# Performance work log

Hardware: AMD Instinct MI355X
Metric: run time of the kernel (lower is better)

The kernel has to match this reference:

```python
import jax, jax.numpy as jnp
import numpy as np

H, D = 4, 128          # num_heads, per-head out dim (= hidden_feats)
IN = 256               # input feature dim for both node types
N_HOST, N_FLOW = 100000, 100000
E1, E2 = 200000, 200000  # edges for host->flow ('h2f') and flow->host ('f2h')
LN_EPS = 1e-5
SLOPE = 0.2            # GATConv default LeakyReLU negative_slope


def setup_inputs() -> dict:
    key = jax.random.key(0)
    ks = jax.random.split(key, 16)
    nrm = lambda k, s, sc=0.05: jax.random.normal(k, s, jnp.float32) * sc
    return {
        'feat_host': jax.random.normal(ks[0], (N_HOST, IN), jnp.float32),
        'feat_flow': jax.random.normal(ks[1], (N_FLOW, IN), jnp.float32),
        # GATConv params for rel h2f (src=host, dst=flow)
        'W1': nrm(ks[2], (IN, H * D)), 'al1': nrm(ks[3], (H, D)), 'ar1': nrm(ks[4], (H, D)), 'b1': jnp.zeros((H * D,), jnp.float32),
        # GATConv params for rel f2h (src=flow, dst=host)
        'W2': nrm(ks[5], (IN, H * D)), 'al2': nrm(ks[6], (H, D)), 'ar2': nrm(ks[7], (H, D)), 'b2': jnp.zeros((H * D,), jnp.float32),
        # residual projections (in_feats 256 != hidden 128)
        'projW_host': nrm(ks[8], (IN, D)), 'projb_host': jnp.zeros((D,), jnp.float32),
        'projW_flow': nrm(ks[9], (IN, D)), 'projb_flow': jnp.zeros((D,), jnp.float32),
        # LayerNorm params
        'g_host': jnp.ones((D,), jnp.float32), 'be_host': jnp.zeros((D,), jnp.float32),
        'g_flow': jnp.ones((D,), jnp.float32), 'be_flow': jnp.zeros((D,), jnp.float32),
        # edge lists
        'e1_src': jax.random.randint(ks[10], (E1,), 0, N_HOST, jnp.int32),
        'e1_dst': jax.random.randint(ks[11], (E1,), 0, N_FLOW, jnp.int32),
        'e2_src': jax.random.randint(ks[12], (E2,), 0, N_FLOW, jnp.int32),
        'e2_dst': jax.random.randint(ks[13], (E2,), 0, N_HOST, jnp.int32),
    }


def _gat_rel(h_src, h_dst, src, dst, W, al, ar, b, n_dst):
    """DGL GATConv (shared fc, residual=False, bias=True, eval-mode dropout)."""
    fs = (h_src @ W).reshape(-1, H, D)                     # [Ns,H,D]
    fd = (h_dst @ W).reshape(-1, H, D)                     # [Nd,H,D]
    el = jnp.sum(fs * al, axis=-1)                         # [Ns,H]
    er = jnp.sum(fd * ar, axis=-1)                         # [Nd,H]
    e = jax.nn.leaky_relu(el[src] + er[dst], SLOPE)        # [E,H]
    # edge softmax over incoming edges of each dst node (per head), max-stabilized
    m = jax.ops.segment_max(e, dst, num_segments=n_dst)    # [Nd,H]
    ee = jnp.exp(e - m[dst])
    s = jax.ops.segment_sum(ee, dst, num_segments=n_dst)   # [Nd,H]
    a = ee / s[dst]                                        # [E,H]
    msg = a[:, :, None] * fs[src]                          # [E,H,D]
    rst = jax.ops.segment_sum(msg, dst, num_segments=n_dst)  # [Nd,H,D]
    return rst + b.reshape(H, D)


def _tail(agg, feat, pW, pb, g, be):
    """mean over heads -> residual(projected) -> LayerNorm -> GELU (dropout=eval)."""
    h = agg.mean(axis=1)                                   # [N,D]
    c = h + (feat @ pW + pb)
    mu = c.mean(axis=-1, keepdims=True)
    var = ((c - mu) ** 2).mean(axis=-1, keepdims=True)
    y = (c - mu) / jnp.sqrt(var + LN_EPS) * g + be
    return jax.nn.gelu(y, approximate=False)


def reference(feat_host, feat_flow, W1, al1, ar1, b1, W2, al2, ar2, b2,
              projW_host, projb_host, projW_flow, projb_flow,
              g_host, be_host, g_flow, be_flow,
              e1_src, e1_dst, e2_src, e2_dst):
    flow_agg = _gat_rel(feat_host, feat_flow, e1_src, e1_dst, W1, al1, ar1, b1, N_FLOW)
    host_agg = _gat_rel(feat_flow, feat_host, e2_src, e2_dst, W2, al2, ar2, b2, N_HOST)
    host_out = _tail(host_agg, feat_host, projW_host, projb_host, g_host, be_host)
    flow_out = _tail(flow_agg, feat_flow, projW_flow, projb_flow, g_flow, be_flow)
    return host_out, flow_out
```

## Files before the change

kernel.cpp:

```cpp
#include <hip/hip_runtime.h>
#include <math.h>

#define NN 100000
#define EE 200000
#define HH 4
#define DD 128
#define HD 512
#define KIN 256
#define LN_EPS 1e-5f
#define SLOPE 0.2f
#define NB_SCAN 98

#define CSW(a) ((a) ^ (((a) >> 5) & 31))

typedef short bf16x8 __attribute__((ext_vector_type(8)));
typedef unsigned short u16x4 __attribute__((ext_vector_type(4)));
typedef float f32x4 __attribute__((ext_vector_type(4)));

typedef __attribute__((address_space(3))) unsigned int lds_uint;
typedef const __attribute__((address_space(1))) unsigned int glb_uint;

static __device__ __forceinline__ void gload_lds16(const void* g, void* l) {
  __builtin_amdgcn_global_load_lds((glb_uint*)g, (lds_uint*)l, 16, 0, 0);
}

static __device__ __forceinline__ unsigned short f2bf(float x) {
  unsigned int u = __float_as_uint(x);
  u += 0x7fffu + ((u >> 16) & 1u);
  return (unsigned short)(u >> 16);
}
static __device__ __forceinline__ float bf_lo(unsigned int u) {
  return __uint_as_float(u << 16);
}
static __device__ __forceinline__ float bf_hi(unsigned int u) {
  return __uint_as_float(u & 0xffff0000u);
}

static __device__ __forceinline__ float erf_fast(float x) {
  float ax = fabsf(x);
  float t = __builtin_amdgcn_rcpf(fmaf(0.3275911f, ax, 1.0f));
  float p = fmaf(1.061405429f, t, -1.453152027f);
  p = fmaf(p, t, 1.421413741f);
  p = fmaf(p, t, -0.284496736f);
  p = fmaf(p, t, 0.254829592f);
  p = p * t;
  float r = 1.0f - p * __expf(-ax * ax);
  return copysignf(r, x);
}
static __device__ __forceinline__ float gelu_fast(float y) {
  return 0.5f * y * (1.0f + erf_fast(y * 0.70710678118f));
}

__global__ __launch_bounds__(256) void convw(
    const float* __restrict__ W1, const float* __restrict__ W2,
    const float* __restrict__ pWh, const float* __restrict__ pWf,
    short* __restrict__ W1t, short* __restrict__ W2t,
    short* __restrict__ pWht, short* __restrict__ pWft) {
  int idx = blockIdx.x * 256 + threadIdx.x;
  if (idx < 512 * 256) {
    int n = idx >> 8, k = idx & 255;
    W1t[idx] = (short)f2bf(W1[(size_t)k * HD + n]);
    W2t[idx] = (short)f2bf(W2[(size_t)k * HD + n]);
  }
  if (idx < 128 * 256) {
    int n = idx >> 8, k = idx & 255;
    pWht[idx] = (short)f2bf(pWh[(size_t)k * DD + n]);
    pWft[idx] = (short)f2bf(pWf[(size_t)k * DD + n]);
  }
}

__global__ __launch_bounds__(256) void make_c(
    const float* __restrict__ W1, const float* __restrict__ al1, const float* __restrict__ ar1,
    const float* __restrict__ W2, const float* __restrict__ al2, const float* __restrict__ ar2,
    float* __restrict__ Cout) {
  int which = blockIdx.y;
  const float* W = (which < 2) ? W1 : W2;
  const float* a = (which == 0) ? al1 : (which == 1) ? ar1 : (which == 2) ? al2 : ar2;
  int k = threadIdx.x;
  float* C = Cout + (size_t)which * 1024;
#pragma unroll
  for (int h = 0; h < HH; h++) {
    float s = 0.f;
    for (int d = 0; d < DD; d++) s = fmaf(W[(size_t)k * HD + h * DD + d], a[h * DD + d], s);
    C[k * HH + h] = s;
  }
}

__global__ __launch_bounds__(256) void make_bm(
    const float* __restrict__ b1, const float* __restrict__ pbf,
    const float* __restrict__ b2, const float* __restrict__ pbh,
    float* __restrict__ bm) {
  int d = threadIdx.x;
  if (d < 128) {
    bm[d] = 0.25f * (b1[d] + b1[128 + d] + b1[256 + d] + b1[384 + d]) + pbf[d];
  } else {
    int dd = d - 128;
    bm[d] = 0.25f * (b2[dd] + b2[128 + dd] + b2[256 + dd] + b2[384 + dd]) + pbh[dd];
  }
}

__global__ __launch_bounds__(256) void prep_feat(
    const float* __restrict__ X, const float* __restrict__ C1, const float* __restrict__ C2,
    short* __restrict__ Xb, float* __restrict__ o1, float* __restrict__ o2, int M) {
  __shared__ float Cs[KIN * 8];
  int tid = threadIdx.x;
  for (int i = tid; i < KIN * 4; i += 256) {
    int k = i >> 2, h = i & 3;
    Cs[CSW(k * 8 + h)] = C1[i];
    Cs[CSW(k * 8 + 4 + h)] = C2[i];
  }
  __syncthreads();
  int wave = tid >> 6, lane = tid & 63;
  int n = blockIdx.x * 4 + wave;
  if (n >= M) return;
  float4 xv = ((const float4*)(X + (size_t)n * KIN))[lane];
  float xs[4] = {xv.x, xv.y, xv.z, xv.w};
  u16x4 pk;
  pk[0] = f2bf(xs[0]); pk[1] = f2bf(xs[1]); pk[2] = f2bf(xs[2]); pk[3] = f2bf(xs[3]);
  *(u16x4*)(Xb + (size_t)n * KIN + lane * 4) = pk;
  float acc[8] = {0.f, 0.f, 0.f, 0.f, 0.f, 0.f, 0.f, 0.f};
#pragma unroll
  for (int j = 0; j < 4; j++) {
    int k = lane * 4 + j;
#pragma unroll
    for (int t = 0; t < 8; t++) acc[t] = fmaf(xs[j], Cs[CSW(k * 8 + t)], acc[t]);
  }
#pragma unroll
  for (int off = 32; off >= 1; off >>= 1)
#pragma unroll
    for (int t = 0; t < 8; t++) acc[t] += __shfl_xor(acc[t], off);
  if (lane == 0) {
#pragma unroll
    for (int h = 0; h < HH; h++) {
      o1[(size_t)n * HH + h] = acc[h];
      o2[(size_t)n * HH + h] = acc[4 + h];
    }
  }
}

__global__ __launch_bounds__(256) void skinny8(
    const float* __restrict__ X, const float* __restrict__ C1, const float* __restrict__ C2,
    float* __restrict__ o1, float* __restrict__ o2, int M) {
  __shared__ float Cs[KIN * 8];
  int tid = threadIdx.x;
  for (int i = tid; i < KIN * 4; i += 256) {
    int k = i >> 2, h = i & 3;
    Cs[CSW(k * 8 + h)] = C1[i];
    Cs[CSW(k * 8 + 4 + h)] = C2[i];
  }
  __syncthreads();
  int wave = tid >> 6, lane = tid & 63;
  int n = blockIdx.x * 4 + wave;
  if (n >= M) return;
  float4 xv = ((const float4*)(X + (size_t)n * KIN))[lane];
  float xs[4] = {xv.x, xv.y, xv.z, xv.w};
  float acc[8] = {0.f, 0.f, 0.f, 0.f, 0.f, 0.f, 0.f, 0.f};
#pragma unroll
  for (int j = 0; j < 4; j++) {
    int k = lane * 4 + j;
#pragma unroll
    for (int t = 0; t < 8; t++) acc[t] = fmaf(xs[j], Cs[CSW(k * 8 + t)], acc[t]);
  }
#pragma unroll
  for (int off = 32; off >= 1; off >>= 1)
#pragma unroll
    for (int t = 0; t < 8; t++) acc[t] += __shfl_xor(acc[t], off);
  if (lane == 0) {
#pragma unroll
    for (int h = 0; h < HH; h++) {
      o1[(size_t)n * HH + h] = acc[h];
      o2[(size_t)n * HH + h] = acc[4 + h];
    }
  }
}

__global__ __launch_bounds__(256) void hist2(
    const int* __restrict__ d1, const int* __restrict__ d2,
    int* __restrict__ c1, int* __restrict__ c2) {
  int gid = blockIdx.x * 256 + threadIdx.x;
  if (gid < EE) atomicAdd(&c1[d1[gid]], 1);
  else if (gid < 2 * EE) atomicAdd(&c2[d2[gid - EE]], 1);
}

__global__ __launch_bounds__(256) void scan_chunk(
    const int* __restrict__ c1, const int* __restrict__ c2,
    int* __restrict__ rp1, int* __restrict__ rp2, int* __restrict__ bsum) {
  int rel = blockIdx.y;
  const int* counts = rel ? c2 : c1;
  int* rowptr = rel ? rp2 : rp1;
  int* bs = bsum + rel * 128;
  __shared__ int sd[256];
  int tid = threadIdx.x;
  int base = blockIdx.x * 1024 + tid * 4;
  int c[4];
#pragma unroll
  for (int j = 0; j < 4; j++) c[j] = (base + j < NN) ? counts[base + j] : 0;
  int tot = c[0] + c[1] + c[2] + c[3];
  sd[tid] = tot; __syncthreads();
  for (int o = 1; o < 256; o <<= 1) {
    int v = (tid >= o) ? sd[tid - o] : 0;
    __syncthreads();
    sd[tid] += v;
    __syncthreads();
  }
  int excl = sd[tid] - tot;
  int run = excl;
#pragma unroll
  for (int j = 0; j < 4; j++) {
    if (base + j < NN) rowptr[base + j] = run;
    run += c[j];
  }
  if (tid == 255) bs[blockIdx.x] = sd[255];
}

__global__ __launch_bounds__(128) void scan_bsum(int* __restrict__ bsum) {
  int rel = blockIdx.y;
  int* bs = bsum + rel * 128;
  __shared__ int sd[128];
  int tid = threadIdx.x;
  int v = (tid < NB_SCAN) ? bs[tid] : 0;
  sd[tid] = v; __syncthreads();
  for (int o = 1; o < 128; o <<= 1) {
    int t = (tid >= o) ? sd[tid - o] : 0;
    __syncthreads();
    sd[tid] += t;
    __syncthreads();
  }
  bs[tid] = sd[tid] - v;
}

__global__ __launch_bounds__(256) void addoff2(
    int* __restrict__ rp1, int* __restrict__ rp2,
    int* __restrict__ cur1, int* __restrict__ cur2,
    const int* __restrict__ bsum) {
  int rel = blockIdx.y;
  int* rowptr = rel ? rp2 : rp1;
  int* cur = rel ? cur2 : cur1;
  const int* bs = bsum + rel * 128;
  int i = blockIdx.x * 256 + threadIdx.x;
  if (i < NN) {
    int r = rowptr[i] + bs[i >> 10];
    rowptr[i] = r;
    cur[i] = r;
  }
  if (i == 0) rowptr[NN] = EE;
}

__global__ __launch_bounds__(256) void fill_s(
    const int* __restrict__ e1s, const int* __restrict__ e1d,
    const int* __restrict__ e2s, const int* __restrict__ e2d,
    const float* __restrict__ el1, const float* __restrict__ er1,
    const float* __restrict__ el2, const float* __restrict__ er2,
    int* __restrict__ cur1, int* __restrict__ cur2,
    int* __restrict__ adj1, int* __restrict__ adj2,
    float* __restrict__ wexp1, float* __restrict__ wexp2) {
  int gid = blockIdx.x * 256 + threadIdx.x;
  int rel = (gid >= EE);
  if (gid >= 2 * EE) return;
  int e = rel ? gid - EE : gid;
  const int* srcp = rel ? e2s : e1s;
  const int* dstp = rel ? e2d : e1d;
  const float* el = rel ? el2 : el1;
  const float* er = rel ? er2 : er1;
  int* cur = rel ? cur2 : cur1;
  int* adj = rel ? adj2 : adj1;
  float* wexp = rel ? wexp2 : wexp1;
  int si = srcp[e], di = dstp[e];
  int p = atomicAdd(&cur[di], 1);
  adj[p] = si;
  float4 l = *(const float4*)(el + (size_t)si * HH);
  float4 r = *(const float4*)(er + (size_t)di * HH);
  float v0 = l.x + r.x, v1 = l.y + r.y, v2 = l.z + r.z, v3 = l.w + r.w;
  v0 = v0 > 0.f ? v0 : SLOPE * v0; v1 = v1 > 0.f ? v1 : SLOPE * v1;
  v2 = v2 > 0.f ? v2 : SLOPE * v2; v3 = v3 > 0.f ? v3 : SLOPE * v3;
  *(float4*)(wexp + (size_t)p * HH) =
      make_float4(__expf(v0), __expf(v1), __expf(v2), __expf(v3));
}

template <int ABF>
__global__ __launch_bounds__(256) void mfma_gemm(
    const void* __restrict__ Av, const short* __restrict__ Wt,
    void* __restrict__ Cout, int ldC, int M, int write_bf, int ncol) {
  __shared__ short As[128 * 64];
  __shared__ short Bs[128 * 64];
  int nwg = gridDim.x;
  int q = nwg >> 3, r = nwg & 7;
  int xcd = blockIdx.x & 7, seq = blockIdx.x >> 3;
  int lid = (xcd < r) ? (xcd * (q + 1) + seq) : (r * (q + 1) + (xcd - r) * q + seq);
  int row0 = (lid / ncol) * 128;
  int col0 = (lid % ncol) * 128;

  int tid = threadIdx.x;
  int lane = tid & 63, wid = tid >> 6;
  int wm = wid >> 1, wn = wid & 1;

  f32x4 acc[4][4];
#pragma unroll
  for (int i = 0; i < 4; i++)
#pragma unroll
    for (int j = 0; j < 4; j++) acc[i][j] = (f32x4){0.f, 0.f, 0.f, 0.f};

  int am = tid >> 1;
  int akh = (tid & 1) * 32;
  bool arow_ok = (row0 + am) < M;

  for (int k0 = 0; k0 < KIN; k0 += 64) {
    __syncthreads();
    if (ABF) {
      int rr8 = lane >> 3;
      int bby = (lane & 7) * 16;
#pragma unroll
      for (int c2 = 0; c2 < 4; c2++) {
        int rr = wid * 32 + c2 * 8 + rr8;
        int rg = row0 + rr; if (rg > M - 1) rg = M - 1;
        int sb = bby ^ ((rr & 7) << 4);
        gload_lds16((const char*)Av + (size_t)rg * (KIN * 2) + k0 * 2 + sb,
                    (char*)As + wid * 4096 + c2 * 1024);
      }
#pragma unroll
      for (int c2 = 0; c2 < 4; c2++) {
        int rr = wid * 32 + c2 * 8 + rr8;
        int sb = bby ^ ((rr & 7) << 4);
        gload_lds16((const char*)Wt + (size_t)(col0 + rr) * (KIN * 2) + k0 * 2 + sb,
                    (char*)Bs + wid * 4096 + c2 * 1024);
      }
    } else {
      const float* xp = (const float*)Av + (size_t)(row0 + am) * KIN + k0 + akh;
#pragma unroll
      for (int c = 0; c < 4; c++) {
        float4 v0, v1;
        if (arow_ok) {
          v0 = *(const float4*)(xp + c * 8);
          v1 = *(const float4*)(xp + c * 8 + 4);
        } else {
          v0 = make_float4(0.f, 0.f, 0.f, 0.f);
          v1 = v0;
        }
        bf16x8 pk;
        pk[0] = (short)f2bf(v0.x); pk[1] = (short)f2bf(v0.y);
        pk[2] = (short)f2bf(v0.z); pk[3] = (short)f2bf(v0.w);
        pk[4] = (short)f2bf(v1.x); pk[5] = (short)f2bf(v1.y);
        pk[6] = (short)f2bf(v1.z); pk[7] = (short)f2bf(v1.w);
        int kc = akh + c * 8;
        int ad = (am * 128 + kc * 2) ^ ((am & 7) << 4);
        *(bf16x8*)((char*)As + ad) = pk;
      }
      int bn = tid >> 1;
      int bkh = (tid & 1) * 32;
      const short* wp = Wt + (size_t)(col0 + bn) * KIN + k0 + bkh;
#pragma unroll
      for (int c = 0; c < 4; c++) {
        bf16x8 pv = *(const bf16x8*)(wp + c * 8);
        int kc = bkh + c * 8;
        int bd = (bn * 128 + kc * 2) ^ ((bn & 7) << 4);
        *(bf16x8*)((char*)Bs + bd) = pv;
      }
    }
    __syncthreads();
#pragma unroll
    for (int ks = 0; ks < 2; ks++) {
      int kb = ks * 32 + (lane >> 4) * 8;
      bf16x8 af[4], bfv[4];
#pragma unroll
      for (int mf = 0; mf < 4; mf++) {
        int rr = wm * 64 + mf * 16 + (lane & 15);
        int ad = (rr * 128 + kb * 2) ^ ((rr & 7) << 4);
        af[mf] = *(bf16x8*)((char*)As + ad);
      }
#pragma unroll
      for (int nf = 0; nf < 4; nf++) {
        int cc = wn * 64 + nf * 16 + (lane & 15);
        int bd = (cc * 128 + kb * 2) ^ ((cc & 7) << 4);
        bfv[nf] = *(bf16x8*)((char*)Bs + bd);
      }
#pragma unroll
      for (int mf = 0; mf < 4; mf++)
#pragma unroll
        for (int nf = 0; nf < 4; nf++)
          acc[mf][nf] = __builtin_amdgcn_mfma_f32_16x16x32_bf16(af[mf], bfv[nf], acc[mf][nf], 0, 0, 0);
    }
  }
  int lr = lane >> 4, lc = lane & 15;
#pragma unroll
  for (int mf = 0; mf < 4; mf++) {
#pragma unroll
    for (int r4 = 0; r4 < 4; r4++) {
      int row = row0 + wm * 64 + mf * 16 + lr * 4 + r4;
      if (row < M) {
#pragma unroll
        for (int nf = 0; nf < 4; nf++) {
          int col = col0 + wn * 64 + nf * 16 + lc;
          float v = acc[mf][nf][r4];
          if (write_bf) ((unsigned short*)Cout)[(size_t)row * ldC + col] = f2bf(v);
          else ((float*)Cout)[(size_t)row * ldC + col] = v;
        }
      }
    }
  }
}

__global__ __launch_bounds__(256) void agg2(
    const int* __restrict__ rowptr, const int* __restrict__ adj,
    const float* __restrict__ wexp,
    const unsigned short* __restrict__ fsb,
    const float* __restrict__ bm,
    const float* __restrict__ g, const float* __restrict__ be,
    float* __restrict__ out, int M) {
  int wave = threadIdx.x >> 6, lane = threadIdx.x & 63;
  int n = blockIdx.x * 4 + wave;
  if (n >= M) return;
  int beg = rowptr[n], end = rowptr[n + 1];
  int lh = lane >> 4, lc = lane & 15;
  float sh = 0.f;
  float m[8] = {0.f, 0.f, 0.f, 0.f, 0.f, 0.f, 0.f, 0.f};
  for (int t = beg; t < end; t++) {
    int si = adj[t];
    float wh = wexp[(size_t)t * HH + lh];
    sh += wh;
    uint4 u = *(const uint4*)(fsb + (size_t)si * HD + lane * 8);
    m[0] = fmaf(wh, bf_lo(u.x), m[0]); m[1] = fmaf(wh, bf_hi(u.x), m[1]);
    m[2] = fmaf(wh, bf_lo(u.y), m[2]); m[3] = fmaf(wh, bf_hi(u.y), m[3]);
    m[4] = fmaf(wh, bf_lo(u.z), m[4]); m[5] = fmaf(wh, bf_hi(u.z), m[5]);
    m[6] = fmaf(wh, bf_lo(u.w), m[6]); m[7] = fmaf(wh, bf_hi(u.w), m[7]);
  }
  float rsh = sh > 0.f ? 0.25f / sh : 0.f;
#pragma unroll
  for (int j = 0; j < 8; j++) m[j] *= rsh;
#pragma unroll
  for (int j = 0; j < 8; j++) {
    m[j] += __shfl_xor(m[j], 16);
    m[j] += __shfl_xor(m[j], 32);
  }
  const float4* bmp = (const float4*)(bm + lc * 8);
  float4 b0 = bmp[0], b1 = bmp[1];
  const float4* orow = (const float4*)(out + (size_t)n * DD + lc * 8);
  float4 p0 = orow[0], p1 = orow[1];
  float c[8];
  c[0] = m[0] + b0.x + p0.x; c[1] = m[1] + b0.y + p0.y;
  c[2] = m[2] + b0.z + p0.z; c[3] = m[3] + b0.w + p0.w;
  c[4] = m[4] + b1.x + p1.x; c[5] = m[5] + b1.y + p1.y;
  c[6] = m[6] + b1.z + p1.z; c[7] = m[7] + b1.w + p1.w;
  float ss = c[0] + c[1] + c[2] + c[3] + c[4] + c[5] + c[6] + c[7];
  ss += __shfl_xor(ss, 1); ss += __shfl_xor(ss, 2);
  ss += __shfl_xor(ss, 4); ss += __shfl_xor(ss, 8);
  float mu = ss * (1.f / 128.f);
  float vv = 0.f;
#pragma unroll
  for (int j = 0; j < 8; j++) { float d = c[j] - mu; vv = fmaf(d, d, vv); }
  vv += __shfl_xor(vv, 1); vv += __shfl_xor(vv, 2);
  vv += __shfl_xor(vv, 4); vv += __shfl_xor(vv, 8);
  float inv = rsqrtf(vv * (1.f / 128.f) + LN_EPS);
  const float4* gp = (const float4*)(g + lc * 8);
  const float4* bep = (const float4*)(be + lc * 8);
  float4 g0 = gp[0], g1 = gp[1];
  float4 e0 = bep[0], e1 = bep[1];
  float gv[8] = {g0.x, g0.y, g0.z, g0.w, g1.x, g1.y, g1.z, g1.w};
  float ev[8] = {e0.x, e0.y, e0.z, e0.w, e1.x, e1.y, e1.z, e1.w};
  float o[8];
#pragma unroll
  for (int j = 0; j < 8; j++) {
    float y = (c[j] - mu) * inv * gv[j] + ev[j];
    o[j] = gelu_fast(y);
  }
  if (lane < 16) {
    float4* op = (float4*)(out + (size_t)n * DD + lane * 8);
    op[0] = make_float4(o[0], o[1], o[2], o[3]);
    op[1] = make_float4(o[4], o[5], o[6], o[7]);
  }
}

extern "C" void kernel_launch(void* const* d_in, const int* in_sizes, int n_in,
                              void* d_out, int out_size, void* d_ws, size_t ws_size,
                              hipStream_t stream) {
  const float* feat_host = (const float*)d_in[0];
  const float* feat_flow = (const float*)d_in[1];
  const float* W1  = (const float*)d_in[2];
  const float* al1 = (const float*)d_in[3];
  const float* ar1 = (const float*)d_in[4];
  const float* b1  = (const float*)d_in[5];
  const float* W2  = (const float*)d_in[6];
  const float* al2 = (const float*)d_in[7];
  const float* ar2 = (const float*)d_in[8];
  const float* b2  = (const float*)d_in[9];
  const float* pWh = (const float*)d_in[10];
  const float* pbh = (const float*)d_in[11];
  const float* pWf = (const float*)d_in[12];
  const float* pbf = (const float*)d_in[13];
  const float* gh  = (const float*)d_in[14];
  const float* beh = (const float*)d_in[15];
  const float* gf  = (const float*)d_in[16];
  const float* bef = (const float*)d_in[17];
  const int* e1s = (const int*)d_in[18];
  const int* e1d = (const int*)d_in[19];
  const int* e2s = (const int*)d_in[20];
  const int* e2d = (const int*)d_in[21];

  float* out = (float*)d_out;
  float* host_out = out;
  float* flow_out = out + (size_t)NN * DD;

  float* ws = (float*)d_ws;
  size_t off = 0;
  unsigned short* fsb = (unsigned short*)(ws + off); off += (size_t)NN * 256;
  short* W1t  = (short*)(ws + off); off += (512 * 256) / 2;
  short* W2t  = (short*)(ws + off); off += (512 * 256) / 2;
  short* pWht = (short*)(ws + off); off += (128 * 256) / 2;
  short* pWft = (short*)(ws + off); off += (128 * 256) / 2;
  float* el1b = ws + off; off += (size_t)NN * HH;
  float* er1b = ws + off; off += (size_t)NN * HH;
  float* el2b = ws + off; off += (size_t)NN * HH;
  float* er2b = ws + off; off += (size_t)NN * HH;
  float* Cbuf = ws + off; off += 4096;
  float* bm   = ws + off; off += 256;
  float* wexp1 = ws + off; off += (size_t)EE * HH;
  float* wexp2 = ws + off; off += (size_t)EE * HH;
  int* rp1  = (int*)(ws + off);
  int* rp2  = rp1 + (NN + 1);
  int* adj1 = rp2 + (NN + 1);
  int* adj2 = adj1 + EE;
  int* bsum = adj2 + EE;
  int* cur1 = bsum + 256;
  int* cur2 = cur1 + NN;
  off += (size_t)(2 * (NN + 1) + 2 * EE + 256 + 2 * NN + 4);
  size_t base_bytes = (off + 1024) * sizeof(float);
  size_t featb_bytes = (size_t)NN * KIN * 2 * 2;
  bool use_featb = ws_size >= base_bytes + featb_bytes;
  short* fhb = nullptr;
  short* ffb = nullptr;
  if (use_featb) {
    fhb = (short*)(ws + off); off += (size_t)NN * KIN / 2;
    ffb = (short*)(ws + off); off += (size_t)NN * KIN / 2;
  }

  dim3 blk(256);
  int gx = (NN + 127) / 128;
  int pf_g = (NN + 3) / 4;
  int ag_g = (NN + 3) / 4;
  int ee2_g = (2 * EE + 255) / 256;
  int nn_g = (NN + 255) / 256;

  convw<<<512, blk, 0, stream>>>(W1, W2, pWh, pWf, W1t, W2t, pWht, pWft);
  make_c<<<dim3(1, 4), blk, 0, stream>>>(W1, al1, ar1, W2, al2, ar2, Cbuf);
  make_bm<<<1, blk, 0, stream>>>(b1, pbf, b2, pbh, bm);
  if (use_featb) {
    prep_feat<<<pf_g, blk, 0, stream>>>(feat_host, Cbuf + 0,    Cbuf + 3072, fhb, el1b, er2b, NN);
    prep_feat<<<pf_g, blk, 0, stream>>>(feat_flow, Cbuf + 1024, Cbuf + 2048, ffb, er1b, el2b, NN);
  } else {
    skinny8<<<pf_g, blk, 0, stream>>>(feat_host, Cbuf + 0,    Cbuf + 3072, el1b, er2b, NN);
    skinny8<<<pf_g, blk, 0, stream>>>(feat_flow, Cbuf + 1024, Cbuf + 2048, er1b, el2b, NN);
  }

  hipMemsetAsync(cur1, 0, (size_t)2 * NN * sizeof(int), stream);
  hist2<<<ee2_g, blk, 0, stream>>>(e1d, e2d, cur1, cur2);
  scan_chunk<<<dim3(NB_SCAN, 2), blk, 0, stream>>>(cur1, cur2, rp1, rp2, bsum);
  scan_bsum<<<dim3(1, 2), 128, 0, stream>>>(bsum);
  addoff2<<<dim3(nn_g, 2), blk, 0, stream>>>(rp1, rp2, cur1, cur2, bsum);
  fill_s<<<ee2_g, blk, 0, stream>>>(e1s, e1d, e2s, e2d, el1b, er1b, el2b, er2b,
                                    cur1, cur2, adj1, adj2, wexp1, wexp2);

  if (use_featb) {
    mfma_gemm<1><<<gx, blk, 0, stream>>>(ffb, pWft, flow_out, DD, NN, 0, 1);
    mfma_gemm<1><<<gx * 4, blk, 0, stream>>>(fhb, W1t, fsb, HD, NN, 1, 4);
  } else {
    mfma_gemm<0><<<gx, blk, 0, stream>>>(feat_flow, pWft, flow_out, DD, NN, 0, 1);
    mfma_gemm<0><<<gx * 4, blk, 0, stream>>>(feat_host, W1t, fsb, HD, NN, 1, 4);
  }
  agg2<<<ag_g, blk, 0, stream>>>(rp1, adj1, wexp1, fsb, bm, gf, bef, flow_out, NN);

  if (use_featb) {
    mfma_gemm<1><<<gx, blk, 0, stream>>>(fhb, pWht, host_out, DD, NN, 0, 1);
    mfma_gemm<1><<<gx * 4, blk, 0, stream>>>(ffb, W2t, fsb, HD, NN, 1, 4);
  } else {
    mfma_gemm<0><<<gx, blk, 0, stream>>>(feat_host, pWht, host_out, DD, NN, 0, 1);
    mfma_gemm<0><<<gx * 4, blk, 0, stream>>>(feat_flow, W2t, fsb, HD, NN, 1, 4);
  }
  agg2<<<ag_g, blk, 0, stream>>>(rp2, adj2, wexp2, fsb, bm + 128, gh, beh, host_out, NN);
}
```

Baseline: 537.0 us.

## Compute attention logits with MFMA in fused bf16 feature-conversion kernel

Replaces the per-row wave-reduction kernel that converted features to bf16 and computed the el/er attention logits with an MFMA-based kernel. The logit coefficient matrix is precomputed in bf16, transposed and zero-padded to 16 columns. Each wave handles 16 rows and uses 16x16x32 bf16 MFMAs. Both node types are processed in one launch via blockIdx.y. This removes the LDS staging and shuffle reductions, but the logits now use bf16-rounded inputs and coefficients, which costs some precision.

After: 476.5 us. 11.3% less time.

```diff
diff --git a/kernel.cpp b/kernel.cpp
--- a/kernel.cpp
+++ b/kernel.cpp
@@ -72,7 +72,7 @@
 __global__ __launch_bounds__(256) void make_c(
     const float* __restrict__ W1, const float* __restrict__ al1, const float* __restrict__ ar1,
     const float* __restrict__ W2, const float* __restrict__ al2, const float* __restrict__ ar2,
-    float* __restrict__ Cout) {
+    float* __restrict__ Cout, short* __restrict__ CtH, short* __restrict__ CtF) {
   int which = blockIdx.y;
   const float* W = (which < 2) ? W1 : W2;
   const float* a = (which == 0) ? al1 : (which == 1) ? ar1 : (which == 2) ? al2 : ar2;
@@ -83,6 +83,18 @@
     float s = 0.f;
     for (int d = 0; d < DD; d++) s = fmaf(W[(size_t)k * HD + h * DD + d], a[h * DD + d], s);
     C[k * HH + h] = s;
+    short b = (short)f2bf(s);
+    if (which == 0)      CtH[h * KIN + k] = b;
+    else if (which == 3) CtH[(4 + h) * KIN + k] = b;
+    else if (which == 1) CtF[h * KIN + k] = b;
+    else                 CtF[(4 + h) * KIN + k] = b;
+  }
+  if (which == 0) {
+#pragma unroll
+    for (int j = 0; j < 8; j++) CtH[(8 + j) * KIN + k] = 0;
+  } else if (which == 1) {
+#pragma unroll
+    for (int j = 0; j < 8; j++) CtF[(8 + j) * KIN + k] = 0;
   }
 }
 
@@ -99,41 +111,52 @@
   }
 }
 
-__global__ __launch_bounds__(256) void prep_feat(
-    const float* __restrict__ X, const float* __restrict__ C1, const float* __restrict__ C2,
-    short* __restrict__ Xb, float* __restrict__ o1, float* __restrict__ o2, int M) {
-  __shared__ float Cs[KIN * 8];
-  int tid = threadIdx.x;
-  for (int i = tid; i < KIN * 4; i += 256) {
-    int k = i >> 2, h = i & 3;
-    Cs[CSW(k * 8 + h)] = C1[i];
-    Cs[CSW(k * 8 + 4 + h)] = C2[i];
-  }
-  __syncthreads();
-  int wave = tid >> 6, lane = tid & 63;
-  int n = blockIdx.x * 4 + wave;
-  if (n >= M) return;
-  float4 xv = ((const float4*)(X + (size_t)n * KIN))[lane];
-  float xs[4] = {xv.x, xv.y, xv.z, xv.w};
-  u16x4 pk;
-  pk[0] = f2bf(xs[0]); pk[1] = f2bf(xs[1]); pk[2] = f2bf(xs[2]); pk[3] = f2bf(xs[3]);
-  *(u16x4*)(Xb + (size_t)n * KIN + lane * 4) = pk;
-  float acc[8] = {0.f, 0.f, 0.f, 0.f, 0.f, 0.f, 0.f, 0.f};
-#pragma unroll
-  for (int j = 0; j < 4; j++) {
-    int k = lane * 4 + j;
-#pragma unroll
-    for (int t = 0; t < 8; t++) acc[t] = fmaf(xs[j], Cs[CSW(k * 8 + t)], acc[t]);
-  }
-#pragma unroll
-  for (int off = 32; off >= 1; off >>= 1)
-#pragma unroll
-    for (int t = 0; t < 8; t++) acc[t] += __shfl_xor(acc[t], off);
-  if (lane == 0) {
-#pragma unroll
-    for (int h = 0; h < HH; h++) {
-      o1[(size_t)n * HH + h] = acc[h];
-      o2[(size_t)n * HH + h] = acc[4 + h];
+__global__ __launch_bounds__(256) void prep_mfma(
+    const float* __restrict__ XH, const float* __restrict__ XF,
+    const short* __restrict__ CtH, const short* __restrict__ CtF,
+    short* __restrict__ XbH, short* __restrict__ XbF,
+    float* __restrict__ o1H, float* __restrict__ o2H,
+    float* __restrict__ o1F, float* __restrict__ o2F, int M) {
+  int which = blockIdx.y;
+  const float* X = which ? XF : XH;
+  const short* Ct = which ? CtF : CtH;
+  short* Xb = which ? XbF : XbH;
+  float* o1 = which ? o1F : o1H;
+  float* o2 = which ? o2F : o2H;
+  int tid = threadIdx.x, lane = tid & 63, wid = tid >> 6;
+  int row0 = blockIdx.x * 64 + wid * 16;
+  if (row0 >= M) return;
+  int lr = lane & 15, lk = lane >> 4;
+  bf16x8 bfrag[8];
+#pragma unroll
+  for (int kc = 0; kc < 8; kc++)
+    bfrag[kc] = *(const bf16x8*)(Ct + lr * KIN + kc * 32 + lk * 8);
+  int arow = row0 + lr;
+  if (arow > M - 1) arow = M - 1;
+  const float* xp = X + (size_t)arow * KIN + lk * 8;
+  short* xbp = Xb + (size_t)arow * KIN + lk * 8;
+  f32x4 acc = (f32x4){0.f, 0.f, 0.f, 0.f};
+#pragma unroll
+  for (int kc = 0; kc < 8; kc++) {
+    float4 v0 = *(const float4*)(xp + kc * 32);
+    float4 v1 = *(const float4*)(xp + kc * 32 + 4);
+    bf16x8 af;
+    af[0] = (short)f2bf(v0.x); af[1] = (short)f2bf(v0.y);
+    af[2] = (short)f2bf(v0.z); af[3] = (short)f2bf(v0.w);
+    af[4] = (short)f2bf(v1.x); af[5] = (short)f2bf(v1.y);
+    af[6] = (short)f2bf(v1.z); af[7] = (short)f2bf(v1.w);
+    *(bf16x8*)(xbp + kc * 32) = af;
+    acc = __builtin_amdgcn_mfma_f32_16x16x32_bf16(af, bfrag[kc], acc, 0, 0, 0);
+  }
+  if (lr < 8) {
+    int rbase = row0 + lk * 4;
+#pragma unroll
+    for (int r = 0; r < 4; r++) {
+      int row = rbase + r;
+      if (row < M) {
+        if (lr < 4) o1[(size_t)row * HH + lr] = acc[r];
+        else        o2[(size_t)row * HH + (lr - 4)] = acc[r];
+      }
     }
   }
 }
@@ -511,6 +534,8 @@
   float* el2b = ws + off; off += (size_t)NN * HH;
   float* er2b = ws + off; off += (size_t)NN * HH;
   float* Cbuf = ws + off; off += 4096;
+  short* CtH  = (short*)(ws + off); off += 2048;
+  short* CtF  = (short*)(ws + off); off += 2048;
   float* bm   = ws + off; off += 256;
   float* wexp1 = ws + off; off += (size_t)EE * HH;
   float* wexp2 = ws + off; off += (size_t)EE * HH;
@@ -534,20 +559,22 @@
 
   dim3 blk(256);
   int gx = (NN + 127) / 128;
-  int pf_g = (NN + 3) / 4;
+  int pm_g = (NN + 63) / 64;
+  int sk_g = (NN + 3) / 4;
   int ag_g = (NN + 3) / 4;
   int ee2_g = (2 * EE + 255) / 256;
   int nn_g = (NN + 255) / 256;
 
   convw<<<512, blk, 0, stream>>>(W1, W2, pWh, pWf, W1t, W2t, pWht, pWft);
-  make_c<<<dim3(1, 4), blk, 0, stream>>>(W1, al1, ar1, W2, al2, ar2, Cbuf);
+  make_c<<<dim3(1, 4), blk, 0, stream>>>(W1, al1, ar1, W2, al2, ar2, Cbuf, CtH, CtF);
   make_bm<<<1, blk, 0, stream>>>(b1, pbf, b2, pbh, bm);
   if (use_featb) {
-    prep_feat<<<pf_g, blk, 0, stream>>>(feat_host, Cbuf + 0,    Cbuf + 3072, fhb, el1b, er2b, NN);
-    prep_feat<<<pf_g, blk, 0, stream>>>(feat_flow, Cbuf + 1024, Cbuf + 2048, ffb, er1b, el2b, NN);
+    prep_mfma<<<dim3(pm_g, 2), blk, 0, stream>>>(
+        feat_host, feat_flow, CtH, CtF, fhb, ffb,
+        el1b, er2b, er1b, el2b, NN);
   } else {
-    skinny8<<<pf_g, blk, 0, stream>>>(feat_host, Cbuf + 0,    Cbuf + 3072, el1b, er2b, NN);
-    skinny8<<<pf_g, blk, 0, stream>>>(feat_flow, Cbuf + 1024, Cbuf + 2048, er1b, el2b, NN);
+    skinny8<<<sk_g, blk, 0, stream>>>(feat_host, Cbuf + 0,    Cbuf + 3072, el1b, er2b, NN);
+    skinny8<<<sk_g, blk, 0, stream>>>(feat_flow, Cbuf + 1024, Cbuf + 2048, er1b, el2b, NN);
   }
 
   hipMemsetAsync(cur1, 0, (size_t)2 * NN * sizeof(int), stream);
```
